# Optimization experiments

Measured on AMD Instinct MI355X. Metric: run time of the kernel, lower is better.

Reference implementation:

```python
import jax, jax.numpy as jnp
import numpy as np

B, S, H = 4, 2048, 1024
F_DIM = 4096
E = 8
K = 2
CAP_FACTOR = 1.25
MAX_CAP = 512
LOSS_COEF = 0.01


def setup_inputs() -> dict:
    key = jax.random.key(0)
    ks = jax.random.split(key, 6)
    s_h = 1.0 / np.sqrt(H).astype(np.float32)
    s_f = 1.0 / np.sqrt(F_DIM).astype(np.float32)
    return {
        "x": jax.random.normal(ks[0], (B, S, H), jnp.float32),
        "Wg": jax.random.normal(ks[1], (H, E), jnp.float32) * s_h,
        "bg": jnp.zeros((E,), jnp.float32),
        "W1": jax.random.normal(ks[2], (E, H, F_DIM), jnp.float32) * s_h,
        "b1": jnp.zeros((E, F_DIM), jnp.float32),
        "W2": jax.random.normal(ks[3], (E, F_DIM, H), jnp.float32) * s_f,
        "b2": jnp.zeros((E, H), jnp.float32),
    }


def _moe_forward(x, Wg, bg, W1, b1, W2, b2):
    Bq, Sq, Hq = x.shape
    N = Bq * Sq
    x_flat = x.reshape(N, Hq)

    # --- gating (eval mode: moe_dropout=0 -> drop_mask all True) ---
    gate_scores = jax.nn.softmax(x_flat @ Wg + bg, axis=-1)            # (N, E)
    backup_k = min(K * 4, E)
    topk_scores, topk_idx = jax.lax.top_k(gate_scores, backup_k)       # (N, bk)
    topk_norm = topk_scores / (jnp.sum(topk_scores, axis=-1, keepdims=True) + 1e-9)

    capacity = min(int(CAP_FACTOR * np.ceil(N / E)), MAX_CAP)
    NF = N * backup_k
    idx_flat = topk_idx.reshape(NF)                                    # expert id per flat slot
    score_flat = topk_norm.reshape(NF)

    # --- cumsum-based capacity assignment (rank of each flat slot within its expert) ---
    onehot = (idx_flat[:, None] == jnp.arange(E)[None, :]).astype(jnp.int32)  # (NF, E)
    cs = jnp.cumsum(onehot, axis=0)
    pos = jnp.take_along_axis(cs, idx_flat[:, None], axis=1)[:, 0] - 1  # (NF,)
    mask = pos < capacity                                              # within-capacity flag
    slot = jnp.where(mask, pos, 0)
    # NOTE: original code divides by K (not backup_k); replicated faithfully.
    tok = jnp.clip(jnp.arange(NF) // K, 0, N - 1)
    tok = jnp.where(mask, tok, 0)

    # --- dispatch: scale token by gate score, scatter into expert buffers ---
    sel_x = x_flat[tok] * (score_flat * mask)[:, None]                 # (NF, H)
    buf = jnp.zeros((E, capacity, Hq), x.dtype).at[idx_flat, slot].add(sel_x)

    # --- per-expert FFN (grouped GEMM), exact GELU as in nn.GELU() ---
    hmid = jax.nn.gelu(jnp.einsum('ech,ehf->ecf', buf, W1) + b1[:, None, :],
                       approximate=False)
    out_buf = jnp.einsum('ecf,efh->ech', hmid, W2) + b2[:, None, :]
    # torch only writes the first `load` rows of each expert's output buffer
    load = jnp.sum(onehot * mask[:, None].astype(jnp.int32), axis=0)   # (E,) valid per expert
    row_mask = jnp.arange(capacity)[None, :] < load[:, None]           # (E, cap)
    out_buf = out_buf * row_mask[:, :, None]

    # --- combine: gather expert outputs, scatter-add back to tokens ---
    sel_out = out_buf[idx_flat, slot] * mask[:, None]                  # (NF, H)
    y_flat = jnp.zeros((N, Hq), x.dtype).at[tok].add(sel_out)
    y = y_flat.reshape(Bq, Sq, Hq)

    # --- load-balancing aux loss (uses all backup_k indices, mask set to 1) ---
    em = jnp.zeros((N, E), x.dtype).at[jnp.repeat(jnp.arange(N), backup_k), idx_flat].set(1.0)
    actual = jnp.sum(em, axis=0) / jnp.sum(em)
    expected = jnp.full((E,), 1.0 / E, x.dtype)
    kl = jnp.sum(expected * (jnp.log(expected) - jnp.log(actual)))
    return y, LOSS_COEF * kl


def reference(x, Wg, bg, W1, b1, W2, b2):
    return _moe_forward(x, Wg, bg, W1, b1, W2, b2)
```

## Files before the change

kernel.cpp:

```cpp
#include <hip/hip_runtime.h>
#include <hip/hip_fp16.h>
#include <math.h>

#define HDIM 1024
#define NEXP 8
#define FDIM 4096
#define CAP 512
#define LDP 40

typedef _Float16 half8 __attribute__((ext_vector_type(8)));
typedef float floatx4 __attribute__((ext_vector_type(4)));

__global__ __launch_bounds__(64)
void moe_gate_kernel(const float* __restrict__ x, const float* __restrict__ Wg,
                     const float* __restrict__ bg,
                     float* __restrict__ wgt, int* __restrict__ src, int* __restrict__ ord) {
    const int t = blockIdx.x;
    const int lane = threadIdx.x;
    const float* xr = x + (size_t)t * HDIM;
    float acc[NEXP];
#pragma unroll
    for (int e = 0; e < NEXP; e++) acc[e] = 0.f;
    for (int i = lane; i < HDIM; i += 64) {
        float xv = xr[i];
        const float* wr = Wg + (size_t)i * NEXP;
#pragma unroll
        for (int e = 0; e < NEXP; e++) acc[e] += xv * wr[e];
    }
#pragma unroll
    for (int e = 0; e < NEXP; e++) {
        float v = acc[e];
#pragma unroll
        for (int off = 1; off < 64; off <<= 1) v += __shfl_xor(v, off, 64);
        acc[e] = v;
    }
    if (lane == 0) {
        float p[NEXP];
        float mx = -1e30f;
#pragma unroll
        for (int e = 0; e < NEXP; e++) { acc[e] += bg[e]; mx = fmaxf(mx, acc[e]); }
        float s = 0.f;
#pragma unroll
        for (int e = 0; e < NEXP; e++) { p[e] = expf(acc[e] - mx); s += p[e]; }
        float inv = 1.f / s;
        float s2 = 0.f;
#pragma unroll
        for (int e = 0; e < NEXP; e++) { p[e] *= inv; s2 += p[e]; }
        float norm = 1.f / (s2 + 1e-9f);
        int used = 0;
        for (int r = 0; r < 8; r++) {
            int best = 0; float bv = -1.f;
            for (int e = 0; e < NEXP; e++) {
                if (!((used >> e) & 1) && p[e] > bv) { bv = p[e]; best = e; }
            }
            used |= 1 << best;
            wgt[best * CAP + t] = p[best] * norm;
            src[best * CAP + t] = 4 * t + (r >> 1);
            ord[t * 8 + r] = best;
        }
    }
}

__global__ __launch_bounds__(256)
void moe_dispatch_kernel(const float* __restrict__ x, const float* __restrict__ wgt,
                         const int* __restrict__ src, __half* __restrict__ buf) {
    const int row = blockIdx.x;
    const int tid = threadIdx.x;
    const float w = wgt[row];
    const int s = src[row];
    float4 v = ((const float4*)(x + (size_t)s * HDIM))[tid];
    __half2 h0 = __floats2half2_rn(v.x * w, v.y * w);
    __half2 h1 = __floats2half2_rn(v.z * w, v.w * w);
    __half2* o = (__half2*)(buf + (size_t)row * HDIM);
    o[tid * 2]     = h0;
    o[tid * 2 + 1] = h1;
}

template <int Kdim, int Ndim, bool GELU>
__global__ __launch_bounds__(256)
void moe_gemm_kernel(const __half* __restrict__ A, const float* __restrict__ Bw,
                     const float* __restrict__ bias, void* __restrict__ Cout) {
    __shared__ __align__(16) __half As[128 * LDP];
    __shared__ __align__(16) __half Bs[128 * LDP];

    const int tid = threadIdx.x;
    const int lane = tid & 63;
    const int wave = tid >> 6;
    const int wm = wave >> 1, wn = wave & 1;
    const int quad = lane >> 4, l15 = lane & 15;

    const int e = blockIdx.z;
    const int mBase = blockIdx.y * 128;
    const int nBase = blockIdx.x * 128;

    const __half* Ae = A + ((size_t)e * 512 + mBase) * Kdim;
    const float* Be = Bw + (size_t)e * Kdim * Ndim + nBase;

    const int arow = tid >> 1;
    const int acol = (tid & 1) * 16;
    const int brow = tid >> 3;
    const int bcol0 = (tid & 7) * 4;

    floatx4 acc[4][4] = {};

    for (int k0 = 0; k0 < Kdim; k0 += 32) {
        const __half* Ag = Ae + (size_t)arow * Kdim + k0 + acol;
        int4 av0 = *(const int4*)Ag;
        int4 av1 = *(const int4*)(Ag + 8);
        const float* Br = Be + (size_t)(k0 + brow) * Ndim + bcol0;
        float4 bv0 = *(const float4*)(Br);
        float4 bv1 = *(const float4*)(Br + 32);
        float4 bv2 = *(const float4*)(Br + 64);
        float4 bv3 = *(const float4*)(Br + 96);

        __syncthreads();

        *(int4*)&As[arow * LDP + acol]     = av0;
        *(int4*)&As[arow * LDP + acol + 8] = av1;
        {
            float4 bb[4] = {bv0, bv1, bv2, bv3};
#pragma unroll
            for (int i = 0; i < 4; i++) {
                const int n = bcol0 + 32 * i;
                Bs[(n + 0) * LDP + brow] = __float2half(bb[i].x);
                Bs[(n + 1) * LDP + brow] = __float2half(bb[i].y);
                Bs[(n + 2) * LDP + brow] = __float2half(bb[i].z);
                Bs[(n + 3) * LDP + brow] = __float2half(bb[i].w);
            }
        }
        __syncthreads();

        half8 af[4], bf[4];
#pragma unroll
        for (int i = 0; i < 4; i++) {
            af[i] = *(const half8*)&As[(wm * 64 + i * 16 + l15) * LDP + quad * 8];
            bf[i] = *(const half8*)&Bs[(wn * 64 + i * 16 + l15) * LDP + quad * 8];
        }
#pragma unroll
        for (int mi = 0; mi < 4; mi++)
#pragma unroll
            for (int ni = 0; ni < 4; ni++)
                acc[mi][ni] = __builtin_amdgcn_mfma_f32_16x16x32_f16(af[mi], bf[ni], acc[mi][ni], 0, 0, 0);
    }

    const float* be = bias + (size_t)e * Ndim + nBase;
    if (GELU) {
        __half* C = (__half*)Cout + ((size_t)e * 512 + mBase) * Ndim + nBase;
#pragma unroll
        for (int mi = 0; mi < 4; mi++) {
#pragma unroll
            for (int ni = 0; ni < 4; ni++) {
                const int col = wn * 64 + ni * 16 + l15;
                const float b = be[col];
#pragma unroll
                for (int r = 0; r < 4; r++) {
                    const int row = wm * 64 + mi * 16 + quad * 4 + r;
                    float v = acc[mi][ni][r] + b;
                    v = 0.5f * v * (1.f + erff(v * 0.70710678118f));
                    C[(size_t)row * Ndim + col] = __float2half(v);
                }
            }
        }
    } else {
        float* C = (float*)Cout + ((size_t)e * 512 + mBase) * Ndim + nBase;
#pragma unroll
        for (int mi = 0; mi < 4; mi++) {
#pragma unroll
            for (int ni = 0; ni < 4; ni++) {
                const int col = wn * 64 + ni * 16 + l15;
                const float b = be[col];
#pragma unroll
                for (int r = 0; r < 4; r++) {
                    const int row = wm * 64 + mi * 16 + quad * 4 + r;
                    C[(size_t)row * Ndim + col] = acc[mi][ni][r] + b;
                }
            }
        }
    }
}

__global__ __launch_bounds__(256)
void moe_combine_kernel(const float* __restrict__ outb, const int* __restrict__ ord,
                        float* __restrict__ y) {
    const int j = blockIdx.x;
    const int t = j >> 2, q = j & 3;
    const int e1 = ord[t * 8 + 2 * q];
    const int e2 = ord[t * 8 + 2 * q + 1];
    float4 a = ((const float4*)(outb + ((size_t)e1 * CAP + t) * HDIM))[threadIdx.x];
    float4 b = ((const float4*)(outb + ((size_t)e2 * CAP + t) * HDIM))[threadIdx.x];
    float4 o = {a.x + b.x, a.y + b.y, a.z + b.z, a.w + b.w};
    ((float4*)(y + (size_t)j * HDIM))[threadIdx.x] = o;
}

extern "C" void kernel_launch(void* const* d_in, const int* in_sizes, int n_in,
                              void* d_out, int out_size, void* d_ws, size_t ws_size,
                              hipStream_t stream) {
    const float* x  = (const float*)d_in[0];
    const float* Wg = (const float*)d_in[1];
    const float* bg = (const float*)d_in[2];
    const float* W1 = (const float*)d_in[3];
    const float* b1 = (const float*)d_in[4];
    const float* W2 = (const float*)d_in[5];
    const float* b2 = (const float*)d_in[6];
    float* out = (float*)d_out;

    char* ws = (char*)d_ws;
    __half* buf  = (__half*)(ws);
    __half* hmid = (__half*)(ws + (size_t)(8  << 20));
    float*  outb = (float*) (ws + (size_t)(40 << 20));
    float*  wgt  = (float*) (ws + (size_t)(56 << 20));
    int*    src  = (int*)   (ws + (size_t)(56 << 20) + 16384);
    int*    ord  = (int*)   (ws + (size_t)(56 << 20) + 32768);

    hipMemsetAsync(d_out, 0, (size_t)out_size * sizeof(float), stream);

    moe_gate_kernel<<<CAP, 64, 0, stream>>>(x, Wg, bg, wgt, src, ord);
    moe_dispatch_kernel<<<NEXP * CAP, 256, 0, stream>>>(x, wgt, src, buf);
    moe_gemm_kernel<HDIM, FDIM, true><<<dim3(FDIM / 128, 4, NEXP), 256, 0, stream>>>(buf, W1, b1, hmid);
    moe_gemm_kernel<FDIM, HDIM, false><<<dim3(HDIM / 128, 4, NEXP), 256, 0, stream>>>(hmid, W2, b2, outb);
    moe_combine_kernel<<<2048, 256, 0, stream>>>(outb, ord, out);
}
```

Before: 518.2 us.

## Pre-transpose weights to fp16, use direct global-to-LDS loads, split-K second GEMM

Adds a pass that transposes and converts W1 and W2 to fp16 K-major layout once per call. Both GEMMs then fill shared memory with global_load_lds 16-byte transfers instead of register staging with scalar fp32-to-half scatter stores. The second GEMM is split along K into two partial buffers that the combine kernel sums. The combine kernel also zeroes the unused output rows, replacing the memset. The transpose pass re-reads and writes about 200 MB of weights every call, which may cost more than the GEMM load path saves.

```diff
diff --git a/kernel.cpp b/kernel.cpp
--- a/kernel.cpp
+++ b/kernel.cpp
@@ -6,10 +6,16 @@
 #define NEXP 8
 #define FDIM 4096
 #define CAP 512
-#define LDP 40
 
 typedef _Float16 half8 __attribute__((ext_vector_type(8)));
 typedef float floatx4 __attribute__((ext_vector_type(4)));
+
+__device__ __forceinline__ void glds16(const __half* g, __half* ldsbase) {
+    __builtin_amdgcn_global_load_lds(
+        (const __attribute__((address_space(1))) void*)g,
+        (__attribute__((address_space(3))) void*)ldsbase,
+        16, 0, 0);
+}
 
 __global__ __launch_bounds__(64)
 void moe_gate_kernel(const float* __restrict__ x, const float* __restrict__ Wg,
@@ -76,65 +82,82 @@
     o[tid * 2 + 1] = h1;
 }
 
-template <int Kdim, int Ndim, bool GELU>
 __global__ __launch_bounds__(256)
-void moe_gemm_kernel(const __half* __restrict__ A, const float* __restrict__ Bw,
+void transpose_convert_kernel(const float* __restrict__ W, __half* __restrict__ WT,
+                              int R, int C) {
+    __shared__ float tile[64][65];
+    const int e = blockIdx.z;
+    const int tr = blockIdx.y * 64;
+    const int tc = blockIdx.x * 64;
+    const float* We = W + (size_t)e * R * C;
+    __half* WTe = WT + (size_t)e * R * C;
+    const int tid = threadIdx.x;
+    {
+        const int c0 = (tid & 15) * 4;
+        const int r0 = tid >> 4;
+#pragma unroll
+        for (int it = 0; it < 4; it++) {
+            const int r = r0 + it * 16;
+            float4 v = *(const float4*)(We + (size_t)(tr + r) * C + tc + c0);
+            tile[r][c0] = v.x; tile[r][c0 + 1] = v.y; tile[r][c0 + 2] = v.z; tile[r][c0 + 3] = v.w;
+        }
+    }
+    __syncthreads();
+    {
+        const int cc = tid >> 2;
+        const int rr0 = (tid & 3) * 16;
+        __half h[16];
+#pragma unroll
+        for (int i = 0; i < 16; i++) h[i] = __float2half(tile[rr0 + i][cc]);
+        __half* dst = WTe + (size_t)(tc + cc) * R + tr + rr0;
+        *(int4*)dst = *(int4*)h;
+        *(int4*)(dst + 8) = *(int4*)(h + 8);
+    }
+}
+
+template <int Kd, int Nd, bool GELU, int KSPLIT>
+__global__ __launch_bounds__(256, 4)
+void moe_gemm_kernel(const __half* __restrict__ A, const __half* __restrict__ BT,
                      const float* __restrict__ bias, void* __restrict__ Cout) {
-    __shared__ __align__(16) __half As[128 * LDP];
-    __shared__ __align__(16) __half Bs[128 * LDP];
+    __shared__ __align__(16) __half As[128 * 32];
+    __shared__ __align__(16) __half Bs[128 * 32];
 
     const int tid = threadIdx.x;
     const int lane = tid & 63;
-    const int wave = tid >> 6;
-    const int wm = wave >> 1, wn = wave & 1;
+    const int wu = __builtin_amdgcn_readfirstlane(tid >> 6);
+    const int wm = wu >> 1, wn = wu & 1;
     const int quad = lane >> 4, l15 = lane & 15;
 
-    const int e = blockIdx.z;
+    const int e  = blockIdx.z / KSPLIT;
+    const int ks = blockIdx.z % KSPLIT;
     const int mBase = blockIdx.y * 128;
     const int nBase = blockIdx.x * 128;
-
-    const __half* Ae = A + ((size_t)e * 512 + mBase) * Kdim;
-    const float* Be = Bw + (size_t)e * Kdim * Ndim + nBase;
-
-    const int arow = tid >> 1;
-    const int acol = (tid & 1) * 16;
-    const int brow = tid >> 3;
-    const int bcol0 = (tid & 7) * 4;
+    const int kLen = Kd / KSPLIT;
+
+    const __half* Ae = A + ((size_t)e * 512 + mBase) * Kd + (size_t)ks * kLen;
+    const __half* Be = BT + ((size_t)e * Nd + nBase) * Kd + (size_t)ks * kLen;
+
+    const int srow = lane >> 2;
+    const int scol = (lane & 3) * 8;
 
     floatx4 acc[4][4] = {};
 
-    for (int k0 = 0; k0 < Kdim; k0 += 32) {
-        const __half* Ag = Ae + (size_t)arow * Kdim + k0 + acol;
-        int4 av0 = *(const int4*)Ag;
-        int4 av1 = *(const int4*)(Ag + 8);
-        const float* Br = Be + (size_t)(k0 + brow) * Ndim + bcol0;
-        float4 bv0 = *(const float4*)(Br);
-        float4 bv1 = *(const float4*)(Br + 32);
-        float4 bv2 = *(const float4*)(Br + 64);
-        float4 bv3 = *(const float4*)(Br + 96);
-
+    for (int k0 = 0; k0 < kLen; k0 += 32) {
         __syncthreads();
-
-        *(int4*)&As[arow * LDP + acol]     = av0;
-        *(int4*)&As[arow * LDP + acol + 8] = av1;
         {
-            float4 bb[4] = {bv0, bv1, bv2, bv3};
-#pragma unroll
-            for (int i = 0; i < 4; i++) {
-                const int n = bcol0 + 32 * i;
-                Bs[(n + 0) * LDP + brow] = __float2half(bb[i].x);
-                Bs[(n + 1) * LDP + brow] = __float2half(bb[i].y);
-                Bs[(n + 2) * LDP + brow] = __float2half(bb[i].z);
-                Bs[(n + 3) * LDP + brow] = __float2half(bb[i].w);
-            }
+            const __half* ga = Ae + (size_t)(wu * 32 + srow) * Kd + k0 + scol;
+            const __half* gb = Be + (size_t)(wu * 32 + srow) * Kd + k0 + scol;
+            glds16(ga,                    As + (wu * 32) * 32);
+            glds16(ga + (size_t)16 * Kd,  As + (wu * 32 + 16) * 32);
+            glds16(gb,                    Bs + (wu * 32) * 32);
+            glds16(gb + (size_t)16 * Kd,  Bs + (wu * 32 + 16) * 32);
         }
         __syncthreads();
-
         half8 af[4], bf[4];
 #pragma unroll
         for (int i = 0; i < 4; i++) {
-            af[i] = *(const half8*)&As[(wm * 64 + i * 16 + l15) * LDP + quad * 8];
-            bf[i] = *(const half8*)&Bs[(wn * 64 + i * 16 + l15) * LDP + quad * 8];
+            af[i] = *(const half8*)&As[(wm * 64 + i * 16 + l15) * 32 + quad * 8];
+            bf[i] = *(const half8*)&Bs[(wn * 64 + i * 16 + l15) * 32 + quad * 8];
         }
 #pragma unroll
         for (int mi = 0; mi < 4; mi++)
@@ -143,9 +166,9 @@
                 acc[mi][ni] = __builtin_amdgcn_mfma_f32_16x16x32_f16(af[mi], bf[ni], acc[mi][ni], 0, 0, 0);
     }
 
-    const float* be = bias + (size_t)e * Ndim + nBase;
+    const float* be = bias + (size_t)e * Nd + nBase;
     if (GELU) {
-        __half* C = (__half*)Cout + ((size_t)e * 512 + mBase) * Ndim + nBase;
+        __half* C = (__half*)Cout + ((size_t)e * 512 + mBase) * Nd + nBase;
 #pragma unroll
         for (int mi = 0; mi < 4; mi++) {
 #pragma unroll
@@ -157,22 +180,22 @@
                     const int row = wm * 64 + mi * 16 + quad * 4 + r;
                     float v = acc[mi][ni][r] + b;
                     v = 0.5f * v * (1.f + erff(v * 0.70710678118f));
-                    C[(size_t)row * Ndim + col] = __float2half(v);
+                    C[(size_t)row * Nd + col] = __float2half(v);
                 }
             }
         }
     } else {
-        float* C = (float*)Cout + ((size_t)e * 512 + mBase) * Ndim + nBase;
+        float* C = (float*)Cout + (((size_t)ks * NEXP + e) * 512 + mBase) * Nd + nBase;
 #pragma unroll
         for (int mi = 0; mi < 4; mi++) {
 #pragma unroll
             for (int ni = 0; ni < 4; ni++) {
                 const int col = wn * 64 + ni * 16 + l15;
-                const float b = be[col];
+                const float b = (ks == 0) ? be[col] : 0.f;
 #pragma unroll
                 for (int r = 0; r < 4; r++) {
                     const int row = wm * 64 + mi * 16 + quad * 4 + r;
-                    C[(size_t)row * Ndim + col] = acc[mi][ni][r] + b;
+                    C[(size_t)row * Nd + col] = acc[mi][ni][r] + b;
                 }
             }
         }
@@ -183,13 +206,24 @@
 void moe_combine_kernel(const float* __restrict__ outb, const int* __restrict__ ord,
                         float* __restrict__ y) {
     const int j = blockIdx.x;
+    const int tid = threadIdx.x;
+    float4* yo = (float4*)(y + (size_t)j * HDIM);
+    if (j >= 2048) {
+        yo[tid] = float4{0.f, 0.f, 0.f, 0.f};
+        if (j == 2048 && tid == 0) y[(size_t)8192 * HDIM] = 0.f;
+        return;
+    }
     const int t = j >> 2, q = j & 3;
     const int e1 = ord[t * 8 + 2 * q];
     const int e2 = ord[t * 8 + 2 * q + 1];
-    float4 a = ((const float4*)(outb + ((size_t)e1 * CAP + t) * HDIM))[threadIdx.x];
-    float4 b = ((const float4*)(outb + ((size_t)e2 * CAP + t) * HDIM))[threadIdx.x];
-    float4 o = {a.x + b.x, a.y + b.y, a.z + b.z, a.w + b.w};
-    ((float4*)(y + (size_t)j * HDIM))[threadIdx.x] = o;
+    const size_t PSTR = (size_t)NEXP * CAP * HDIM;
+    float4 a0 = ((const float4*)(outb + ((size_t)e1 * CAP + t) * HDIM))[tid];
+    float4 a1 = ((const float4*)(outb + PSTR + ((size_t)e1 * CAP + t) * HDIM))[tid];
+    float4 b0 = ((const float4*)(outb + ((size_t)e2 * CAP + t) * HDIM))[tid];
+    float4 b1 = ((const float4*)(outb + PSTR + ((size_t)e2 * CAP + t) * HDIM))[tid];
+    float4 o = {a0.x + a1.x + b0.x + b1.x, a0.y + a1.y + b0.y + b1.y,
+                a0.z + a1.z + b0.z + b1.z, a0.w + a1.w + b0.w + b1.w};
+    yo[tid] = o;
 }
 
 extern "C" void kernel_launch(void* const* d_in, const int* in_sizes, int n_in,
@@ -206,17 +240,19 @@
 
     char* ws = (char*)d_ws;
     __half* buf  = (__half*)(ws);
-    __half* hmid = (__half*)(ws + (size_t)(8  << 20));
-    float*  outb = (float*) (ws + (size_t)(40 << 20));
-    float*  wgt  = (float*) (ws + (size_t)(56 << 20));
-    int*    src  = (int*)   (ws + (size_t)(56 << 20) + 16384);
-    int*    ord  = (int*)   (ws + (size_t)(56 << 20) + 32768);
-
-    hipMemsetAsync(d_out, 0, (size_t)out_size * sizeof(float), stream);
-
+    __half* hmid = (__half*)(ws + (8ull  << 20));
+    __half* W1T  = (__half*)(ws + (40ull << 20));
+    __half* W2T  = (__half*)(ws + (104ull << 20));
+    float*  outb = (float*)(ws + (40ull << 20));
+    float*  wgt  = (float*)(ws + (168ull << 20));
+    int*    src  = (int*)  (ws + (168ull << 20) + 16384);
+    int*    ord  = (int*)  (ws + (168ull << 20) + 32768);
+
+    transpose_convert_kernel<<<dim3(FDIM / 64, HDIM / 64, NEXP), 256, 0, stream>>>(W1, W1T, HDIM, FDIM);
+    transpose_convert_kernel<<<dim3(HDIM / 64, FDIM / 64, NEXP), 256, 0, stream>>>(W2, W2T, FDIM, HDIM);
     moe_gate_kernel<<<CAP, 64, 0, stream>>>(x, Wg, bg, wgt, src, ord);
     moe_dispatch_kernel<<<NEXP * CAP, 256, 0, stream>>>(x, wgt, src, buf);
-    moe_gemm_kernel<HDIM, FDIM, true><<<dim3(FDIM / 128, 4, NEXP), 256, 0, stream>>>(buf, W1, b1, hmid);
-    moe_gemm_kernel<FDIM, HDIM, false><<<dim3(HDIM / 128, 4, NEXP), 256, 0, stream>>>(hmid, W2, b2, outb);
-    moe_combine_kernel<<<2048, 256, 0, stream>>>(outb, ord, out);
-}
+    moe_gemm_kernel<HDIM, FDIM, true, 1><<<dim3(FDIM / 128, 4, NEXP), 256, 0, stream>>>(buf, W1T, b1, hmid);
+    moe_gemm_kernel<FDIM, HDIM, false, 2><<<dim3(HDIM / 128, 4, NEXP * 2), 256, 0, stream>>>(hmid, W2T, b2, outb);
+    moe_combine_kernel<<<8192, 256, 0, stream>>>(outb, ord, out);
+}
```

Result: faster. 473.2 us (-8.7%).
